# Kernel tuning notes

Measured on AMD Instinct MI355X. Metric: run time of the kernel, lower is better.

## Reference

```python
import jax, jax.numpy as jnp
import numpy as np

B, D, N, F, O = 4096, 256, 128, 128, 256


def setup_inputs() -> dict:
    key = jax.random.key(0)
    ks = jax.random.split(key, 6)
    return {
        "x": jax.random.normal(ks[0], (B, D), dtype=jnp.float32),
        "node_weight": jax.random.normal(ks[1], (N, D + F, F), dtype=jnp.float32),  # torch.randn init
        "node_bias": jax.random.normal(ks[2], (N, F), dtype=jnp.float32),
        "attention": jax.random.normal(ks[3], (N, N), dtype=jnp.float32),
        "out_w": jax.random.normal(ks[4], (F, O), dtype=jnp.float32) * 0.05,  # Linear weight (transposed conv.)
        "out_b": jax.random.normal(ks[5], (O,), dtype=jnp.float32) * 0.05,
        "num_iterations": 3,
    }


def reference(x, node_weight, node_bias, attention, out_w, out_b, num_iterations):
    # connections[i, j] = softmax over j of attention row i
    conn = jax.nn.softmax(attention, axis=1)  # [N, N]
    # Split per-node weight: first F rows act on aggregated states, last D rows on x.
    W_s = node_weight[:, :F, :]   # [N, F, F]
    W_x = node_weight[:, F:, :]   # [N, D, F]
    # x contribution is identical every iteration; precompute once.
    xW = jnp.einsum('bd,ndf->nbf', x, W_x) + node_bias[:, None, :]  # [N, B, F]

    states0 = jnp.zeros((N, B, F), dtype=x.dtype)

    def step(states, _):
        agg = jnp.einsum('ij,jbf->ibf', conn, states)            # attention-weighted aggregation
        new = jax.nn.relu(jnp.einsum('nbf,nfg->nbg', agg, W_s) + xW)
        return new, None

    states, _ = jax.lax.scan(step, states0, None, length=num_iterations)
    final_state = states.mean(axis=0)                            # [B, F]
    return final_state @ out_w + out_b                           # [B, O]
```

## Files before the change

kernel.cpp:

```cpp
#include <hip/hip_runtime.h>

#define DEV __device__ __forceinline__

typedef __attribute__((ext_vector_type(8))) short short8;
typedef __attribute__((ext_vector_type(4))) float floatx4;
typedef __attribute__((ext_vector_type(4))) unsigned short ushort4v;
typedef __attribute__((ext_vector_type(8))) unsigned short ushort8v;

#define Bz 4096
#define Dz 256
#define Nz 128
#define Fz 128
#define Oz 256

static constexpr size_t OFF_CONN = 0;
static constexpr size_t OFF_WT   = 65536;
static constexpr size_t SZ_WT    = (size_t)Nz * 128 * 384 * 2;
static constexpr size_t OFF_OWT  = OFF_WT + SZ_WT;
static constexpr size_t OFF_XB   = OFF_OWT + 65536;
static constexpr size_t OFF_FIN  = OFF_XB + (size_t)Bz * Dz * 2;
static constexpr size_t OFF_ST   = OFF_FIN + (size_t)Bz * Fz * 2;

DEV unsigned short f2bf(float x) {
    unsigned u = __float_as_uint(x);
    u = (u + 0x7FFFu + ((u >> 16) & 1u)) >> 16;
    return (unsigned short)u;
}
DEV float bf2f(unsigned short h) {
    return __uint_as_float(((unsigned)h) << 16);
}

typedef const __attribute__((address_space(1))) void cglobal_void;
typedef __attribute__((address_space(3))) void lds_void;

DEV void gld_lds16(const void* g, void* l) {
    __builtin_amdgcn_global_load_lds((cglobal_void*)g, (lds_void*)l, 16, 0, 0);
}

__global__ __launch_bounds__(64) void k_softmax(const float* __restrict__ att,
                                                unsigned short* __restrict__ conn) {
    int i = blockIdx.x, t = threadIdx.x;
    float a0 = att[i * 128 + t];
    float a1 = att[i * 128 + 64 + t];
    float m = fmaxf(a0, a1);
    for (int o = 32; o > 0; o >>= 1) m = fmaxf(m, __shfl_down(m, o));
    m = __shfl(m, 0);
    float e0 = __expf(a0 - m), e1 = __expf(a1 - m);
    float s = e0 + e1;
    for (int o = 32; o > 0; o >>= 1) s += __shfl_down(s, o);
    s = __shfl(s, 0);
    float inv = 1.f / s;
    conn[i * 128 + t] = f2bf(e0 * inv);
    conn[i * 128 + 64 + t] = f2bf(e1 * inv);
}

__global__ __launch_bounds__(256) void k_transpose(const float* __restrict__ src,
                                                   unsigned short* __restrict__ dst,
                                                   int R, int C, int tilesC,
                                                   long sBatch, long dBatch) {
    __shared__ float ld[32][36];
    int tiles = (R / 32) * tilesC;
    int batch = blockIdx.x / tiles;
    int rem = blockIdx.x % tiles;
    int rt = rem / tilesC, ct = rem % tilesC;
    int t = threadIdx.x;
    int kr = t >> 3, c4 = (t & 7) * 4;
    float4 v = *(const float4*)&src[(size_t)batch * sBatch + (size_t)(rt * 32 + kr) * C + ct * 32 + c4];
    ld[kr][c4 + 0] = v.x; ld[kr][c4 + 1] = v.y; ld[kr][c4 + 2] = v.z; ld[kr][c4 + 3] = v.w;
    __syncthreads();
    int cr = kr, k4 = c4;
    ushort4v o;
    o[0] = f2bf(ld[k4 + 0][cr]);
    o[1] = f2bf(ld[k4 + 1][cr]);
    o[2] = f2bf(ld[k4 + 2][cr]);
    o[3] = f2bf(ld[k4 + 3][cr]);
    *(ushort4v*)&dst[(size_t)batch * dBatch + (size_t)(ct * 32 + cr) * R + rt * 32 + k4] = o;
}

__global__ __launch_bounds__(256) void k_convert(const float* __restrict__ src,
                                                 unsigned short* __restrict__ dst) {
    size_t idx = ((size_t)blockIdx.x * 256 + threadIdx.x) * 4;
    float4 v = *(const float4*)&src[idx];
    ushort4v o;
    o[0] = f2bf(v.x); o[1] = f2bf(v.y); o[2] = f2bf(v.z); o[3] = f2bf(v.w);
    *(ushort4v*)&dst[idx] = o;
}

__global__ __launch_bounds__(256) void k2_agg(const unsigned short* __restrict__ conn,
                                              unsigned short* __restrict__ ST) {
    __shared__ unsigned short lA[128 * 136];
    __shared__ unsigned short lB[2][32 * 128];
    int b = blockIdx.x;
    int t = threadIdx.x, wid = t >> 6, lane = t & 63, q = lane >> 4, cc = lane & 15;
    int wm = (wid >> 1) << 6, wn = (wid & 1) << 6;

#pragma unroll
    for (int it = 0; it < 8; it++) {
        int g = it * 256 + t;
        int row = g >> 4, cg = g & 15;
        *(short8*)&lA[row * 136 + cg * 8] = *(const short8*)&conn[row * 128 + cg * 8];
    }
    floatx4 acc[4][4];
#pragma unroll
    for (int mt = 0; mt < 4; mt++)
#pragma unroll
        for (int nt = 0; nt < 4; nt++) acc[mt][nt] = (floatx4){0.f, 0.f, 0.f, 0.f};

    auto STG = [&](int bufi, int kt) {
#pragma unroll
        for (int it = 0; it < 2; it++) {
            int g = it * 256 + t;
            int j = g >> 4, fg = g & 15;
            int lofs = __builtin_amdgcn_readfirstlane((it * 256 + (wid << 6)) * 8);
            gld_lds16(ST + ((size_t)(kt * 32 + j) * Bz + b) * Fz + fg * 8, &lB[bufi][0] + lofs);
        }
    };
    STG(0, 0);
    STG(1, 1);

#pragma unroll
    for (int kt = 0; kt < 4; kt++) {
        int cur = kt & 1;
        if (kt < 3) asm volatile("s_waitcnt vmcnt(2) lgkmcnt(0)" ::: "memory");
        else        asm volatile("s_waitcnt vmcnt(0) lgkmcnt(0)" ::: "memory");
        __builtin_amdgcn_s_barrier();
        __builtin_amdgcn_sched_barrier(0);
        short8 af[4];
#pragma unroll
        for (int mt = 0; mt < 4; mt++)
            af[mt] = *(const short8*)&lA[(wm + mt * 16 + cc) * 136 + kt * 32 + q * 8];
        short8 bf[4];
#pragma unroll
        for (int nt = 0; nt < 4; nt++) {
            short8 v;
#pragma unroll
            for (int e = 0; e < 8; e++)
                v[e] = (short)lB[cur][(q * 8 + e) * 128 + wn + nt * 16 + cc];
            bf[nt] = v;
        }
#pragma unroll
        for (int mt = 0; mt < 4; mt++)
#pragma unroll
            for (int nt = 0; nt < 4; nt++)
                acc[mt][nt] = __builtin_amdgcn_mfma_f32_16x16x32_bf16(af[mt], bf[nt], acc[mt][nt], 0, 0, 0);
        __builtin_amdgcn_sched_barrier(0);
        __builtin_amdgcn_s_barrier();
        if (kt + 2 < 4) STG(cur, kt + 2);
    }

#pragma unroll
    for (int mt = 0; mt < 4; mt++)
#pragma unroll
        for (int nt = 0; nt < 4; nt++) {
            int f = wn + nt * 16 + cc;
#pragma unroll
            for (int r = 0; r < 4; r++) {
                int il = wm + mt * 16 + q * 4 + r;
                lA[il * 128 + (f ^ ((il & 7) << 3))] = f2bf(acc[mt][nt][r]);
            }
        }
    __syncthreads();
#pragma unroll
    for (int it = 0; it < 8; it++) {
        int idx = it * 256 + t;
        int il = idx >> 4, ch = idx & 15;
        int sch = ch ^ (il & 7);
        ushort8v v = *(const ushort8v*)&lA[il * 128 + sch * 8];
        *(ushort8v*)&ST[((size_t)il * Bz + b) * Fz + ch * 8] = v;
    }
}

template <int KT0>
__global__ __launch_bounds__(256) void k3_fused(unsigned short* __restrict__ ST,
                                                const unsigned short* __restrict__ XB,
                                                const unsigned short* __restrict__ WT,
                                                const float* __restrict__ nb) {
    __shared__ unsigned short lds[2][2][128 * 32];
    int n = blockIdx.x >> 5, bt = blockIdx.x & 31;
    int t = threadIdx.x, wid = t >> 6, lane = t & 63, q = lane >> 4, cc = lane & 15;
    int wm = (wid >> 1) << 6, wn = (wid & 1) << 6;

    const unsigned short* Sg = ST + ((size_t)n * Bz + bt * 128) * Fz;
    const unsigned short* Xg = XB + (size_t)bt * 128 * Dz;
    const unsigned short* Bg = WT + (size_t)n * 128 * 384;

    floatx4 acc[4][4];
#pragma unroll
    for (int mt = 0; mt < 4; mt++)
#pragma unroll
        for (int nt = 0; nt < 4; nt++) acc[mt][nt] = (floatx4){0.f, 0.f, 0.f, 0.f};

    auto STAGE = [&](int bufi, int kt) {
#pragma unroll
        for (int it = 0; it < 2; it++) {
            int g = it * 256 + t;
            int row = g >> 2, kg = g & 3;
            int lofs = __builtin_amdgcn_readfirstlane((it * 256 + (wid << 6)) * 8);
            if (kt < 4)
                gld_lds16(Sg + (size_t)row * Fz + kt * 32 + kg * 8, &lds[bufi][0][0] + lofs);
            else
                gld_lds16(Xg + (size_t)row * Dz + (kt - 4) * 32 + kg * 8, &lds[bufi][0][0] + lofs);
            gld_lds16(Bg + (size_t)row * 384 + kt * 32 + kg * 8, &lds[bufi][1][0] + lofs);
        }
    };
    STAGE(0, KT0);
    STAGE(1, KT0 + 1);

#pragma unroll
    for (int kt = KT0; kt < 12; kt++) {
        int cur = (kt - KT0) & 1;
        if (kt < 11) asm volatile("s_waitcnt vmcnt(4) lgkmcnt(0)" ::: "memory");
        else         asm volatile("s_waitcnt vmcnt(0) lgkmcnt(0)" ::: "memory");
        __builtin_amdgcn_s_barrier();
        __builtin_amdgcn_sched_barrier(0);
        short8 af[4], bfr[4];
#pragma unroll
        for (int mt = 0; mt < 4; mt++)
            af[mt] = *(const short8*)&lds[cur][0][(wm + mt * 16 + cc) * 32 + q * 8];
#pragma unroll
        for (int nt = 0; nt < 4; nt++)
            bfr[nt] = *(const short8*)&lds[cur][1][(wn + nt * 16 + cc) * 32 + q * 8];
#pragma unroll
        for (int mt = 0; mt < 4; mt++)
#pragma unroll
            for (int nt = 0; nt < 4; nt++)
                acc[mt][nt] = __builtin_amdgcn_mfma_f32_16x16x32_bf16(af[mt], bfr[nt], acc[mt][nt], 0, 0, 0);
        __builtin_amdgcn_sched_barrier(0);
        __builtin_amdgcn_s_barrier();
        if (kt + 2 < 12) STAGE(cur, kt + 2);
    }

    unsigned short* outT = &lds[0][0][0];
#pragma unroll
    for (int nt = 0; nt < 4; nt++) {
        int f = wn + nt * 16 + cc;
        float bias = nb[n * Fz + f];
#pragma unroll
        for (int mt = 0; mt < 4; mt++) {
#pragma unroll
            for (int r = 0; r < 4; r++) {
                int bl = wm + mt * 16 + q * 4 + r;
                float v = acc[mt][nt][r] + bias;
                outT[bl * 128 + (f ^ ((bl & 7) << 3))] = f2bf(v > 0.f ? v : 0.f);
            }
        }
    }
    __syncthreads();
    size_t base = ((size_t)n * Bz + (size_t)bt * 128) * Fz;
#pragma unroll
    for (int it = 0; it < 8; it++) {
        int idx = it * 256 + t;
        int bl = idx >> 4, ch = idx & 15;
        int sch = ch ^ (bl & 7);
        ushort8v v = *(const ushort8v*)&outT[bl * 128 + sch * 8];
        *(ushort8v*)&ST[base + (size_t)idx * 8] = v;
    }
}

__global__ __launch_bounds__(256) void k4_mean(const unsigned short* __restrict__ S,
                                               unsigned short* __restrict__ fin) {
    int t = threadIdx.x;
    size_t base = (size_t)blockIdx.x * 2048 + (size_t)t * 8;
    float a[8] = {0.f, 0.f, 0.f, 0.f, 0.f, 0.f, 0.f, 0.f};
    for (int n = 0; n < Nz; n++) {
        ushort8v v = *(const ushort8v*)&S[(size_t)n * Bz * Fz + base];
#pragma unroll
        for (int e = 0; e < 8; e++) a[e] += bf2f(v[e]);
    }
    ushort8v o;
#pragma unroll
    for (int e = 0; e < 8; e++) o[e] = f2bf(a[e] * (1.f / 128.f));
    *(ushort8v*)&fin[base] = o;
}

__global__ __launch_bounds__(256) void k5_out(const unsigned short* __restrict__ fin,
                                              const unsigned short* __restrict__ owt,
                                              const float* __restrict__ ob,
                                              float* __restrict__ out) {
    __shared__ unsigned short lA[128 * 32];
    __shared__ unsigned short lB[128 * 32];
    int bt = blockIdx.x >> 1, ct = blockIdx.x & 1;
    int t = threadIdx.x, wid = t >> 6, lane = t & 63, q = lane >> 4, cc = lane & 15;
    int wm = (wid >> 1) << 6, wn = (wid & 1) << 6;

    const unsigned short* Ag = fin + (size_t)bt * 128 * Fz;
    const unsigned short* Bg = owt + (size_t)ct * 128 * Fz;

    floatx4 acc[4][4];
#pragma unroll
    for (int mt = 0; mt < 4; mt++)
#pragma unroll
        for (int nt = 0; nt < 4; nt++) acc[mt][nt] = (floatx4){0.f, 0.f, 0.f, 0.f};

    for (int kt = 0; kt < 4; kt++) {
#pragma unroll
        for (int it = 0; it < 2; it++) {
            int g = it * 256 + t;
            int row = g >> 2, kg = g & 3;
            int lofs = __builtin_amdgcn_readfirstlane((it * 256 + (wid << 6)) * 8);
            gld_lds16(Ag + (size_t)row * Fz + kt * 32 + kg * 8, lA + lofs);
            gld_lds16(Bg + (size_t)row * Fz + kt * 32 + kg * 8, lB + lofs);
        }
        __syncthreads();
        short8 af[4], bfr[4];
#pragma unroll
        for (int mt = 0; mt < 4; mt++)
            af[mt] = *(const short8*)&lA[(wm + mt * 16 + cc) * 32 + q * 8];
#pragma unroll
        for (int nt = 0; nt < 4; nt++)
            bfr[nt] = *(const short8*)&lB[(wn + nt * 16 + cc) * 32 + q * 8];
#pragma unroll
        for (int mt = 0; mt < 4; mt++)
#pragma unroll
            for (int nt = 0; nt < 4; nt++)
                acc[mt][nt] = __builtin_amdgcn_mfma_f32_16x16x32_bf16(af[mt], bfr[nt], acc[mt][nt], 0, 0, 0);
        __syncthreads();
    }
#pragma unroll
    for (int nt = 0; nt < 4; nt++) {
        int o = ct * 128 + wn + nt * 16 + cc;
        float bias = ob[o];
#pragma unroll
        for (int mt = 0; mt < 4; mt++) {
#pragma unroll
            for (int r = 0; r < 4; r++) {
                int b = bt * 128 + wm + mt * 16 + q * 4 + r;
                out[(size_t)b * Oz + o] = acc[mt][nt][r] + bias;
            }
        }
    }
}

extern "C" void kernel_launch(void* const* d_in, const int* in_sizes, int n_in,
                              void* d_out, int out_size, void* d_ws, size_t ws_size,
                              hipStream_t stream) {
    const float* x = (const float*)d_in[0];
    const float* nw = (const float*)d_in[1];
    const float* nb = (const float*)d_in[2];
    const float* att = (const float*)d_in[3];
    const float* ow = (const float*)d_in[4];
    const float* ob = (const float*)d_in[5];
    char* ws = (char*)d_ws;
    unsigned short* CONN = (unsigned short*)(ws + OFF_CONN);
    unsigned short* WT = (unsigned short*)(ws + OFF_WT);
    unsigned short* OWT = (unsigned short*)(ws + OFF_OWT);
    unsigned short* XB = (unsigned short*)(ws + OFF_XB);
    unsigned short* FIN = (unsigned short*)(ws + OFF_FIN);
    unsigned short* ST = (unsigned short*)(ws + OFF_ST);
    float* out = (float*)d_out;

    k_softmax<<<Nz, 64, 0, stream>>>(att, CONN);
    k_transpose<<<Nz * 48, 256, 0, stream>>>(nw, WT, 384, 128, 4, (long)384 * 128, (long)128 * 384);
    k_transpose<<<32, 256, 0, stream>>>(ow, OWT, 128, 256, 8, 0, 0);
    k_convert<<<(Bz * Dz) / 1024, 256, 0, stream>>>(x, XB);

    k3_fused<4><<<Nz * 32, 256, 0, stream>>>(ST, XB, WT, nb);

    for (int it = 0; it < 2; it++) {
        k2_agg<<<Bz, 256, 0, stream>>>(CONN, ST);
        k3_fused<0><<<Nz * 32, 256, 0, stream>>>(ST, XB, WT, nb);
    }

    k4_mean<<<(Bz * Fz) / 2048, 256, 0, stream>>>(ST, FIN);
    k5_out<<<64, 256, 0, stream>>>(FIN, OWT, ob, out);
}
```

Measured before the change: 404.9 us.

## Enlarge fused GEMM tile to 256 rows with 512 threads and swizzle LDS

The per-node fused GEMM kernel now uses 8 waves and a 256-row batch tile per block, so each staged weight tile is shared by twice as many rows and weight traffic from global memory is halved. LDS staging gets an XOR swizzle on the k-group index to reduce bank conflicts on the fragment reads. The epilogue writes the output in two 128-row halves through the same LDS buffer, which adds extra barriers. The grid is halved, so fewer blocks are resident per CU and occupancy may drop.

```diff
diff --git a/kernel.cpp b/kernel.cpp
--- a/kernel.cpp
+++ b/kernel.cpp
@@ -171,17 +171,17 @@
 }
 
 template <int KT0>
-__global__ __launch_bounds__(256) void k3_fused(unsigned short* __restrict__ ST,
+__global__ __launch_bounds__(512) void k3_fused(unsigned short* __restrict__ ST,
                                                 const unsigned short* __restrict__ XB,
                                                 const unsigned short* __restrict__ WT,
                                                 const float* __restrict__ nb) {
-    __shared__ unsigned short lds[2][2][128 * 32];
-    int n = blockIdx.x >> 5, bt = blockIdx.x & 31;
+    __shared__ unsigned short lds[2][12288];
+    int n = blockIdx.x >> 4, bt = blockIdx.x & 15;
     int t = threadIdx.x, wid = t >> 6, lane = t & 63, q = lane >> 4, cc = lane & 15;
     int wm = (wid >> 1) << 6, wn = (wid & 1) << 6;
 
-    const unsigned short* Sg = ST + ((size_t)n * Bz + bt * 128) * Fz;
-    const unsigned short* Xg = XB + (size_t)bt * 128 * Dz;
+    const unsigned short* Sg = ST + ((size_t)n * Bz + bt * 256) * Fz;
+    const unsigned short* Xg = XB + (size_t)bt * 256 * Dz;
     const unsigned short* Bg = WT + (size_t)n * 128 * 384;
 
     floatx4 acc[4][4];
@@ -193,33 +193,41 @@
     auto STAGE = [&](int bufi, int kt) {
 #pragma unroll
         for (int it = 0; it < 2; it++) {
-            int g = it * 256 + t;
-            int row = g >> 2, kg = g & 3;
-            int lofs = __builtin_amdgcn_readfirstlane((it * 256 + (wid << 6)) * 8);
+            int g = it * 512 + t;
+            int row = g >> 2;
+            int kgs = (g & 3) ^ (row & 3);
+            int lofs = __builtin_amdgcn_readfirstlane((it * 512 + (wid << 6)) * 8);
             if (kt < 4)
-                gld_lds16(Sg + (size_t)row * Fz + kt * 32 + kg * 8, &lds[bufi][0][0] + lofs);
+                gld_lds16(Sg + (size_t)row * Fz + kt * 32 + kgs * 8, &lds[bufi][0] + lofs);
             else
-                gld_lds16(Xg + (size_t)row * Dz + (kt - 4) * 32 + kg * 8, &lds[bufi][0][0] + lofs);
-            gld_lds16(Bg + (size_t)row * 384 + kt * 32 + kg * 8, &lds[bufi][1][0] + lofs);
+                gld_lds16(Xg + (size_t)row * Dz + (kt - 4) * 32 + kgs * 8, &lds[bufi][0] + lofs);
+        }
+        {
+            int row = t >> 2;
+            int kgs = (t & 3) ^ (row & 3);
+            int lofs = __builtin_amdgcn_readfirstlane(8192 + (wid << 6) * 8);
+            gld_lds16(Bg + (size_t)row * 384 + kt * 32 + kgs * 8, &lds[bufi][0] + lofs);
         }
     };
     STAGE(0, KT0);
     STAGE(1, KT0 + 1);
 
+    int sq = (q ^ (cc & 3)) * 8;
+
 #pragma unroll
     for (int kt = KT0; kt < 12; kt++) {
         int cur = (kt - KT0) & 1;
-        if (kt < 11) asm volatile("s_waitcnt vmcnt(4) lgkmcnt(0)" ::: "memory");
+        if (kt < 11) asm volatile("s_waitcnt vmcnt(3) lgkmcnt(0)" ::: "memory");
         else         asm volatile("s_waitcnt vmcnt(0) lgkmcnt(0)" ::: "memory");
         __builtin_amdgcn_s_barrier();
         __builtin_amdgcn_sched_barrier(0);
         short8 af[4], bfr[4];
 #pragma unroll
         for (int mt = 0; mt < 4; mt++)
-            af[mt] = *(const short8*)&lds[cur][0][(wm + mt * 16 + cc) * 32 + q * 8];
+            af[mt] = *(const short8*)&lds[cur][(wm + mt * 16 + cc) * 32 + sq];
 #pragma unroll
         for (int nt = 0; nt < 4; nt++)
-            bfr[nt] = *(const short8*)&lds[cur][1][(wn + nt * 16 + cc) * 32 + q * 8];
+            bfr[nt] = *(const short8*)&lds[cur][8192 + (wn + nt * 16 + cc) * 32 + sq];
 #pragma unroll
         for (int mt = 0; mt < 4; mt++)
 #pragma unroll
@@ -230,30 +238,37 @@
         if (kt + 2 < 12) STAGE(cur, kt + 2);
     }
 
-    unsigned short* outT = &lds[0][0][0];
-#pragma unroll
-    for (int nt = 0; nt < 4; nt++) {
-        int f = wn + nt * 16 + cc;
-        float bias = nb[n * Fz + f];
-#pragma unroll
-        for (int mt = 0; mt < 4; mt++) {
-#pragma unroll
-            for (int r = 0; r < 4; r++) {
-                int bl = wm + mt * 16 + q * 4 + r;
-                float v = acc[mt][nt][r] + bias;
-                outT[bl * 128 + (f ^ ((bl & 7) << 3))] = f2bf(v > 0.f ? v : 0.f);
+    unsigned short* outT = &lds[0][0];
+    size_t base = ((size_t)n * Bz + (size_t)bt * 256) * Fz;
+#pragma unroll
+    for (int h = 0; h < 2; h++) {
+        __syncthreads();
+        if ((wm >> 7) == h) {
+            int bl0 = wm & 127;
+#pragma unroll
+            for (int nt = 0; nt < 4; nt++) {
+                int f = wn + nt * 16 + cc;
+                float bias = nb[n * Fz + f];
+#pragma unroll
+                for (int mt = 0; mt < 4; mt++) {
+#pragma unroll
+                    for (int r = 0; r < 4; r++) {
+                        int bl = bl0 + mt * 16 + q * 4 + r;
+                        float v = acc[mt][nt][r] + bias;
+                        outT[bl * 128 + (f ^ ((bl & 7) << 3))] = f2bf(v > 0.f ? v : 0.f);
+                    }
+                }
             }
         }
-    }
-    __syncthreads();
-    size_t base = ((size_t)n * Bz + (size_t)bt * 128) * Fz;
-#pragma unroll
-    for (int it = 0; it < 8; it++) {
-        int idx = it * 256 + t;
-        int bl = idx >> 4, ch = idx & 15;
-        int sch = ch ^ (bl & 7);
-        ushort8v v = *(const ushort8v*)&outT[bl * 128 + sch * 8];
-        *(ushort8v*)&ST[base + (size_t)idx * 8] = v;
+        __syncthreads();
+#pragma unroll
+        for (int it = 0; it < 4; it++) {
+            int idx = it * 512 + t;
+            int bl = idx >> 4, ch = idx & 15;
+            int sch = ch ^ (bl & 7);
+            ushort8v v = *(const ushort8v*)&outT[bl * 128 + sch * 8];
+            *(ushort8v*)&ST[base + (size_t)h * 128 * Fz + (size_t)idx * 8] = v;
+        }
     }
 }
 
@@ -354,11 +369,11 @@
     k_transpose<<<32, 256, 0, stream>>>(ow, OWT, 128, 256, 8, 0, 0);
     k_convert<<<(Bz * Dz) / 1024, 256, 0, stream>>>(x, XB);
 
-    k3_fused<4><<<Nz * 32, 256, 0, stream>>>(ST, XB, WT, nb);
+    k3_fused<4><<<Nz * 16, 512, 0, stream>>>(ST, XB, WT, nb);
 
     for (int it = 0; it < 2; it++) {
         k2_agg<<<Bz, 256, 0, stream>>>(CONN, ST);
-        k3_fused<0><<<Nz * 32, 256, 0, stream>>>(ST, XB, WT, nb);
+        k3_fused<0><<<Nz * 16, 512, 0, stream>>>(ST, XB, WT, nb);
     }
 
     k4_mean<<<(Bz * Fz) / 2048, 256, 0, stream>>>(ST, FIN);
```

Result: slower. 422.1 us (+4.2%).
